# Kernel optimization log

Hardware: AMD Instinct MI355X
Metric: run time of the kernel (lower is better)

## Reference

```python
import jax, jax.numpy as jnp
import numpy as np
import math

HID = 1152
NH = 16
HD = HID // NH            # 72
P = 2
DEPTH = 4
MLP_M = int(2.0 / 3.0 * int(HID * 4.0))  # 3072 (SwiGLU inner)
FREQ = 256
NCLS = 1000
ROPE_THETA = 10000.0


def rms_norm(x, w, eps=1e-6):
    return x * jax.lax.rsqrt(jnp.mean(jnp.square(x), axis=-1, keepdims=True) + eps) * w


def rotate_half(x):
    # interleaved pairs (a, b) -> (-b, a)
    x2 = x.reshape(x.shape[:-1] + (x.shape[-1] // 2, 2))
    a, b = x2[..., 0], x2[..., 1]
    return jnp.stack((-b, a), axis=-1).reshape(x.shape)


def make_rope(S, head_dim, theta=ROPE_THETA):
    # VisionRotaryEmbedder: per-axis rope dim = head_dim//2, 2 spatial axes concat
    d = head_dim // 2
    f = 1.0 / theta ** (jnp.arange(0, d, 2)[: d // 2].astype(jnp.float32) / d)
    fr = jnp.arange(S, dtype=jnp.float32)[:, None] * f[None, :]   # [S, d//2]
    fr = jnp.repeat(fr, 2, axis=-1)                               # [S, d]
    grid = jnp.concatenate(
        [jnp.broadcast_to(fr[:, None, :], (S, S, d)),
         jnp.broadcast_to(fr[None, :, :], (S, S, d))], axis=-1)   # [S, S, head_dim]
    grid = grid.reshape(S * S, head_dim)
    return jnp.cos(grid), jnp.sin(grid)


def timestep_embedding(t, dim=FREQ, max_period=10000.0):
    half = dim // 2
    freqs = jnp.exp(-math.log(max_period) * jnp.arange(half, dtype=jnp.float32) / half)
    args = t[:, None].astype(jnp.float32) * freqs[None, :]
    return jnp.concatenate([jnp.cos(args), jnp.sin(args)], axis=-1)


def setup_inputs() -> dict:
    key = jax.random.key(0)
    ks = jax.random.split(key, 24)
    s = 0.02
    B, C, H, W = 2, 4, 64, 64
    d = {
        'x': jax.random.normal(ks[0], (B, C, H, W), jnp.float32),
        't': jax.random.uniform(ks[1], (B,), jnp.float32),
        'y': jax.random.randint(ks[2], (B,), 0, NCLS),
        'patch_w': jax.random.normal(ks[3], (P * P * C, HID), jnp.float32) * s,
        'patch_b': jnp.zeros((HID,), jnp.float32),
        't_w1': jax.random.normal(ks[4], (FREQ, HID), jnp.float32) * s,
        't_b1': jnp.zeros((HID,), jnp.float32),
        't_w2': jax.random.normal(ks[5], (HID, HID), jnp.float32) * s,
        't_b2': jnp.zeros((HID,), jnp.float32),
        'y_table': jax.random.normal(ks[6], (NCLS + 1, HID), jnp.float32) * s,
        'norm1_w': jnp.ones((DEPTH, HID), jnp.float32),
        'qkv_w': jax.random.normal(ks[7], (DEPTH, HID, 3 * HID), jnp.float32) * s,
        'qkv_b': jnp.zeros((DEPTH, 3 * HID), jnp.float32),
        'out_w': jax.random.normal(ks[8], (DEPTH, HID, HID), jnp.float32) * s,
        'out_b': jnp.zeros((DEPTH, HID), jnp.float32),
        'norm2_w': jnp.ones((DEPTH, HID), jnp.float32),
        'mlp_w12': jax.random.normal(ks[9], (DEPTH, HID, 2 * MLP_M), jnp.float32) * s,
        'mlp_b12': jnp.zeros((DEPTH, 2 * MLP_M), jnp.float32),
        'mlp_w3': jax.random.normal(ks[10], (DEPTH, MLP_M, HID), jnp.float32) * s,
        'mlp_b3': jnp.zeros((DEPTH, HID), jnp.float32),
        'adaln_w': jax.random.normal(ks[11], (DEPTH, HID, 4 * HID), jnp.float32) * s,
        'adaln_b': jnp.zeros((DEPTH, 4 * HID), jnp.float32),
        'fnorm_w': jnp.ones((HID,), jnp.float32),
        'fadaln_w': jax.random.normal(ks[12], (HID, 2 * HID), jnp.float32) * s,
        'fadaln_b': jnp.zeros((2 * HID,), jnp.float32),
        'flin_w': jax.random.normal(ks[13], (HID, P * P * C), jnp.float32) * s,
        'flin_b': jnp.zeros((P * P * C,), jnp.float32),
    }
    return d


def reference(x, t, y, patch_w, patch_b, t_w1, t_b1, t_w2, t_b2, y_table,
              norm1_w, qkv_w, qkv_b, out_w, out_b, norm2_w,
              mlp_w12, mlp_b12, mlp_w3, mlp_b3, adaln_w, adaln_b,
              fnorm_w, fadaln_w, fadaln_b, flin_w, flin_b):
    B, C, H, W = x.shape
    S = H // P
    L = S * S
    # patchify -> [B, L, P*P*C] -> linear embed
    tok = x.reshape(B, C, S, P, S, P).transpose(0, 2, 4, 3, 5, 1).reshape(B, L, P * P * C)
    h = tok @ patch_w + patch_b
    # conditioning: timestep MLP + class embedding
    temb = timestep_embedding(t)
    temb = jax.nn.silu(temb @ t_w1 + t_b1) @ t_w2 + t_b2
    c = temb + y_table[y]
    c_silu = jax.nn.silu(c)
    cos, sin = make_rope(S, HD)  # [L, HD]
    scale = 1.0 / math.sqrt(HD)

    def block(hx, p):
        n1w, qw, qb, ow, ob, n2w, w12, b12, w3, b3, aw, ab = p
        mod = c_silu @ aw + ab  # [B, 4*HID]
        s_msa, g_msa, s_mlp, g_mlp = jnp.split(mod, 4, axis=-1)
        hmod = rms_norm(hx, n1w) * (1.0 + s_msa[:, None, :])
        qkv = (hmod @ qw + qb).reshape(B, L, 3, NH, HD)
        qkv = jnp.swapaxes(qkv, 1, 3)  # [B, NH, 3, L, HD]
        q, k, v = qkv[:, :, 0], qkv[:, :, 1], qkv[:, :, 2]
        q = q * cos + rotate_half(q) * sin
        k = k * cos + rotate_half(k) * sin
        w = jax.nn.softmax(jnp.einsum('bhqd,bhkd->bhqk', q, k) * scale, axis=-1)
        o = jnp.einsum('bhqk,bhkd->bhqd', w, v)
        o = jnp.swapaxes(o, 1, 2).reshape(B, L, HID) @ ow + ob
        hx = hx + g_msa[:, None, :] * o
        hmod2 = rms_norm(hx, n2w) * (1.0 + s_mlp[:, None, :])
        x12 = hmod2 @ w12 + b12
        x1, x2 = jnp.split(x12, 2, axis=-1)
        m = (jax.nn.silu(x1) * x2) @ w3 + b3
        hx = hx + g_mlp[:, None, :] * m
        return hx, None

    h, _ = jax.lax.scan(block, h, (norm1_w, qkv_w, qkv_b, out_w, out_b, norm2_w,
                                   mlp_w12, mlp_b12, mlp_w3, mlp_b3, adaln_w, adaln_b))

    # final layer: shift+scale modulation then zero-init linear (random here)
    fmod = c_silu @ fadaln_w + fadaln_b
    shift, fscale = jnp.split(fmod, 2, axis=-1)
    hf = rms_norm(h, fnorm_w) * (1.0 + fscale[:, None, :]) + shift[:, None, :]
    out = hf @ flin_w + flin_b  # [B, L, P*P*C]
    out = out.reshape(B, S, S, P, P, C).transpose(0, 5, 1, 3, 2, 4).reshape(B, C, H, W)
    return out
```

## Files before the change

### kernel.cpp

```cpp
#include <hip/hip_runtime.h>
#include <hip/hip_bf16.h>

#define HIDN 1152
#define NHEAD 16
#define HDIM 72
#define LTOK 1024
#define MTOK 2048
#define MLPM 3072

typedef short bf16x8 __attribute__((ext_vector_type(8)));
typedef float f32x4 __attribute__((ext_vector_type(4)));

__device__ __forceinline__ void gload16(const void* g, void* l) {
    __builtin_amdgcn_global_load_lds(
        (const __attribute__((address_space(1))) void*)g,
        (__attribute__((address_space(3))) void*)l,
        16, 0, 0);
}

__global__ __launch_bounds__(256) void k_patch(const float* __restrict__ x,
        const float* __restrict__ pw, const float* __restrict__ pb,
        float* __restrict__ h) {
    int m = blockIdx.x;
    int b = m >> 10, l = m & 1023;
    int si = l >> 5, sj = l & 31;
    __shared__ float toks[16];
    int tid = threadIdx.x;
    if (tid < 16) {
        int pi = tid >> 3, pj = (tid >> 2) & 1, c = tid & 3;
        toks[tid] = x[((size_t)(b*4 + c)*64 + si*2 + pi)*64 + sj*2 + pj];
    }
    __syncthreads();
    for (int o = tid; o < HIDN; o += 256) {
        float acc = pb[o];
        #pragma unroll
        for (int kk = 0; kk < 16; ++kk) acc += toks[kk] * pw[kk*HIDN + o];
        h[(size_t)m*HIDN + o] = acc;
    }
}

__global__ __launch_bounds__(256) void k_temb1_v2(const float* __restrict__ t,
        const float* __restrict__ w1, const float* __restrict__ b1,
        float* __restrict__ temb1) {
    int jt = blockIdx.x, b = blockIdx.y;
    int tid = threadIdx.x;
    __shared__ float emb[256];
    __shared__ float red[128];
    float tv = t[b];
    if (tid < 128) { float f = __expf(-logf(10000.f) * (float)tid / 128.f);        emb[tid] = cosf(tv * f); }
    else           { float f = __expf(-logf(10000.f) * (float)(tid - 128) / 128.f); emb[tid] = sinf(tv * f); }
    __syncthreads();
    int o = jt*128 + (tid & 127), s = tid >> 7;
    float acc = 0.f;
    for (int k = s*128; k < s*128 + 128; ++k) acc += emb[k] * w1[(size_t)k*HIDN + o];
    if (s) red[tid & 127] = acc;
    __syncthreads();
    if (!s) {
        float v = acc + red[tid] + b1[o];
        temb1[b*HIDN + o] = v / (1.f + __expf(-v));
    }
}

__global__ __launch_bounds__(256) void k_csilu_s1(const float* __restrict__ temb1,
        const float* __restrict__ w2, float* __restrict__ csilup) {
    int jt = blockIdx.x, kz = blockIdx.y;
    int tid = threadIdx.x;
    __shared__ float t1s[2][288];
    __shared__ float red[2][128];
    for (int i = tid; i < 576; i += 256)
        t1s[i/288][i%288] = temb1[(i/288)*HIDN + kz*288 + (i%288)];
    __syncthreads();
    int o = jt*128 + (tid & 127), s = tid >> 7;
    float a0 = 0.f, a1 = 0.f;
    for (int i = s*144; i < s*144 + 144; ++i) {
        float wv = w2[(size_t)(kz*288 + i)*HIDN + o];
        a0 += t1s[0][i]*wv; a1 += t1s[1][i]*wv;
    }
    if (s) { red[0][tid & 127] = a0; red[1][tid & 127] = a1; }
    __syncthreads();
    if (!s) {
        csilup[(kz*2 + 0)*HIDN + o] = a0 + red[0][tid];
        csilup[(kz*2 + 1)*HIDN + o] = a1 + red[1][tid];
    }
}

__global__ __launch_bounds__(128) void k_csilu_s2(const float* __restrict__ csilup,
        const float* __restrict__ b2, const float* __restrict__ ytab,
        const int* __restrict__ y, float* __restrict__ csilu) {
    int o = blockIdx.x*128 + threadIdx.x;
    int b = blockIdx.y;
    float acc = b2[o] + ytab[(size_t)y[b]*HIDN + o];
    #pragma unroll
    for (int kz = 0; kz < 4; ++kz) acc += csilup[(kz*2 + b)*HIDN + o];
    csilu[b*HIDN + o] = acc / (1.f + __expf(-acc));
}

__global__ __launch_bounds__(256) void k_cond_s1(const float* __restrict__ csilu,
        const float* __restrict__ adaln_w, const float* __restrict__ fadaln_w,
        float* __restrict__ condp) {
    int ct = blockIdx.x, kz = blockIdx.y;
    int tid = threadIdx.x;
    int c0 = ct*128;
    const float* Wb; int rstride;
    if (c0 < 18432) { int d = c0/4608; Wb = adaln_w + (size_t)d*HIDN*4608 + (c0 % 4608); rstride = 4608; }
    else            { Wb = fadaln_w + (c0 - 18432); rstride = 2304; }
    __shared__ float cs[2][288];
    __shared__ float red[2][128];
    for (int i = tid; i < 576; i += 256)
        cs[i/288][i%288] = csilu[(i/288)*HIDN + kz*288 + (i%288)];
    __syncthreads();
    int o = tid & 127, s = tid >> 7;
    float a0 = 0.f, a1 = 0.f;
    for (int i = s*144; i < s*144 + 144; ++i) {
        float wv = Wb[(size_t)(kz*288 + i)*rstride + o];
        a0 += cs[0][i]*wv; a1 += cs[1][i]*wv;
    }
    if (s) { red[0][o] = a0; red[1][o] = a1; }
    __syncthreads();
    if (!s) {
        condp[((size_t)kz*2 + 0)*20736 + c0 + o] = a0 + red[0][o];
        condp[((size_t)kz*2 + 1)*20736 + c0 + o] = a1 + red[1][o];
    }
}

__global__ __launch_bounds__(256) void k_cond_s2(const float* __restrict__ condp,
        const float* __restrict__ adaln_b, const float* __restrict__ fadaln_b,
        float* __restrict__ modb, float* __restrict__ fmod) {
    int c = blockIdx.x*256 + threadIdx.x;
    int b = blockIdx.y;
    float acc = 0.f;
    #pragma unroll
    for (int kz = 0; kz < 4; ++kz) acc += condp[((size_t)kz*2 + b)*20736 + c];
    if (c < 18432) {
        int d = c/4608, j = c%4608;
        modb[((size_t)d*2 + b)*4608 + j] = acc + adaln_b[(size_t)d*4608 + j];
    } else {
        int j = c - 18432;
        fmod[(size_t)b*2304 + j] = acc + fadaln_b[j];
    }
}

__global__ __launch_bounds__(256) void k_rope(float* __restrict__ cosb, float* __restrict__ sinb) {
    int idx = blockIdx.x*256 + threadIdx.x;
    if (idx >= LTOK*HDIM) return;
    int l = idx / HDIM, dd = idx % HDIM;
    int i = l >> 5, j = l & 31;
    int pos = (dd < 36) ? i : j;
    int mm = ((dd < 36) ? dd : dd - 36) >> 1;
    float f = __expf(-logf(10000.f) * (float)mm / 18.f);
    float fr = (float)pos * f;
    cosb[idx] = cosf(fr);
    sinb[idx] = sinf(fr);
}

__global__ __launch_bounds__(256) void k_rms(const float* __restrict__ hx,
        const float* __restrict__ nw, const float* __restrict__ smod,
        __hip_bfloat16* __restrict__ outp) {
    int m = blockIdx.x; int b = m >> 10;
    int tid = threadIdx.x;
    const float* row = hx + (size_t)m*HIDN;
    float part = 0.f;
    for (int j = tid; j < HIDN; j += 256) { float v = row[j]; part += v*v; }
    for (int off = 32; off; off >>= 1) part += __shfl_xor(part, off);
    __shared__ float wsum[4];
    if ((tid & 63) == 0) wsum[tid >> 6] = part;
    __syncthreads();
    float rs = rsqrtf((wsum[0]+wsum[1]+wsum[2]+wsum[3]) * (1.f/HIDN) + 1e-6f);
    const float* sb = smod + (size_t)b*4608;
    __hip_bfloat16* orow = outp + (size_t)m*HIDN;
    for (int j = tid; j < HIDN; j += 256)
        orow[j] = __float2bfloat16(row[j] * rs * nw[j] * (1.f + sb[j]));
}

__global__ __launch_bounds__(256) void k_castT(const float* __restrict__ W,
        __hip_bfloat16* __restrict__ Wt, int K, int N) {
    __shared__ float tile[32][33];
    int n0 = blockIdx.x*32, k0 = blockIdx.y*32;
    int tx = threadIdx.x, ty = threadIdx.y;
    for (int i = ty; i < 32; i += 8)
        tile[i][tx] = W[(size_t)(k0+i)*N + n0 + tx];
    __syncthreads();
    for (int i = ty; i < 32; i += 8)
        Wt[(size_t)(n0+i)*K + k0 + tx] = __float2bfloat16(tile[tx][i]);
}

template<int EPI, typename OutT>
__global__ __launch_bounds__(256) void k_gemm_bf16(
        const __hip_bfloat16* __restrict__ A,
        const __hip_bfloat16* __restrict__ Wt,
        const float* __restrict__ bias,
        OutT* __restrict__ C, int M, int N, int K,
        const float* __restrict__ gate) {
    __shared__ __hip_bfloat16 Asm[128*64];
    __shared__ __hip_bfloat16 Bsm[128*64];
    int tid = threadIdx.x;
    int lane = tid & 63, w = tid >> 6;
    int wr = w >> 1, wc = w & 1;
    int m0 = blockIdx.y * 128, n0 = blockIdx.x * 128;
    f32x4 acc[4][4] = {};
    int lr = lane >> 3, ls = lane & 7;
    int swz = ls ^ (lr & 7);
    int x7 = lane & 7;
    const __hip_bfloat16* Ag = A  + (size_t)(m0 + lr)*K + swz*8;
    const __hip_bfloat16* Bg = Wt + (size_t)(n0 + lr)*K + swz*8;
    for (int k0 = 0; k0 < K; k0 += 64) {
        #pragma unroll
        for (int i = 0; i < 4; ++i) {
            int seg = w*4 + i;
            gload16(Ag + (size_t)(seg*8)*K + k0, (char*)Asm + seg*1024);
            gload16(Bg + (size_t)(seg*8)*K + k0, (char*)Bsm + seg*1024);
        }
        __syncthreads();
        #pragma unroll
        for (int kk = 0; kk < 2; ++kk) {
            bf16x8 af[4], bfr[4];
            #pragma unroll
            for (int m = 0; m < 4; ++m) {
                int row = wr*64 + m*16 + (lane&15);
                af[m] = *(const bf16x8*)(Asm + row*64 + (((kk*4 + (lane>>4)) ^ x7) * 8));
            }
            #pragma unroll
            for (int n = 0; n < 4; ++n) {
                int col = wc*64 + n*16 + (lane&15);
                bfr[n] = *(const bf16x8*)(Bsm + col*64 + (((kk*4 + (lane>>4)) ^ x7) * 8));
            }
            #pragma unroll
            for (int m = 0; m < 4; ++m)
                #pragma unroll
                for (int n = 0; n < 4; ++n)
                    acc[m][n] = __builtin_amdgcn_mfma_f32_16x16x32_bf16(af[m], bfr[n], acc[m][n], 0, 0, 0);
        }
        __syncthreads();
    }
    int r0 = (lane >> 4) * 4;
    int ccol = lane & 15;
    #pragma unroll
    for (int m = 0; m < 4; ++m) {
        #pragma unroll
        for (int rr = 0; rr < 4; ++rr) {
            int row = m0 + wr*64 + m*16 + r0 + rr;
            int bi = row >> 10;
            #pragma unroll
            for (int n = 0; n < 4; ++n) {
                int col = n0 + wc*64 + n*16 + ccol;
                float val = acc[m][n][rr] + bias[col];
                if (EPI == 0) {
                    C[(size_t)row*N + col] = (OutT)__float2bfloat16(val);
                } else {
                    ((float*)C)[(size_t)row*N + col] += gate[(size_t)bi*4608 + col] * val;
                }
            }
        }
    }
}

__global__ __launch_bounds__(256) void k_gemm64(
        const __hip_bfloat16* __restrict__ A,
        const __hip_bfloat16* __restrict__ Wt,
        const float* __restrict__ bias,
        float* __restrict__ C, int M, int N, int K,
        const float* __restrict__ gate) {
    __shared__ __hip_bfloat16 Asm[64*64];
    __shared__ __hip_bfloat16 Bsm[128*64];
    int tid = threadIdx.x;
    int lane = tid & 63, w = tid >> 6;
    int wr = w >> 1, wc = w & 1;
    int m0 = blockIdx.y * 64, n0 = blockIdx.x * 128;
    f32x4 acc[2][4] = {};
    int lr = lane >> 3, ls = lane & 7;
    int swz = ls ^ (lr & 7);
    int x7 = lane & 7;
    const __hip_bfloat16* Ag = A  + (size_t)(m0 + lr)*K + swz*8;
    const __hip_bfloat16* Bg = Wt + (size_t)(n0 + lr)*K + swz*8;
    for (int k0 = 0; k0 < K; k0 += 64) {
        #pragma unroll
        for (int i = 0; i < 2; ++i) {
            int seg = w*2 + i;
            gload16(Ag + (size_t)(seg*8)*K + k0, (char*)Asm + seg*1024);
        }
        #pragma unroll
        for (int i = 0; i < 4; ++i) {
            int seg = w*4 + i;
            gload16(Bg + (size_t)(seg*8)*K + k0, (char*)Bsm + seg*1024);
        }
        __syncthreads();
        #pragma unroll
        for (int kk = 0; kk < 2; ++kk) {
            bf16x8 af[2], bfr[4];
            #pragma unroll
            for (int m = 0; m < 2; ++m) {
                int row = wr*32 + m*16 + (lane&15);
                af[m] = *(const bf16x8*)(Asm + row*64 + (((kk*4 + (lane>>4)) ^ x7) * 8));
            }
            #pragma unroll
            for (int n = 0; n < 4; ++n) {
                int col = wc*64 + n*16 + (lane&15);
                bfr[n] = *(const bf16x8*)(Bsm + col*64 + (((kk*4 + (lane>>4)) ^ x7) * 8));
            }
            #pragma unroll
            for (int m = 0; m < 2; ++m)
                #pragma unroll
                for (int n = 0; n < 4; ++n)
                    acc[m][n] = __builtin_amdgcn_mfma_f32_16x16x32_bf16(af[m], bfr[n], acc[m][n], 0, 0, 0);
        }
        __syncthreads();
    }
    int r0 = (lane >> 4) * 4;
    int ccol = lane & 15;
    #pragma unroll
    for (int m = 0; m < 2; ++m) {
        #pragma unroll
        for (int rr = 0; rr < 4; ++rr) {
            int row = m0 + wr*32 + m*16 + r0 + rr;
            int bi = row >> 10;
            #pragma unroll
            for (int n = 0; n < 4; ++n) {
                int col = n0 + wc*64 + n*16 + ccol;
                float val = acc[m][n][rr] + bias[col];
                C[(size_t)row*N + col] += gate[(size_t)bi*4608 + col] * val;
            }
        }
    }
}

__global__ __launch_bounds__(256) void k_ropesplit(const __hip_bfloat16* __restrict__ qkv,
        const float* __restrict__ cosb, const float* __restrict__ sinb,
        __hip_bfloat16* __restrict__ q, __hip_bfloat16* __restrict__ k,
        __hip_bfloat16* __restrict__ v) {
    int idx = blockIdx.x*256 + threadIdx.x;
    if (idx >= 2*NHEAD*LTOK*36) return;
    int dp = idx % 36;
    int l  = (idx / 36) % LTOK;
    int h  = (idx / (36*LTOK)) % NHEAD;
    int b  = idx / (36*LTOK*NHEAD);
    int d0 = dp*2;
    size_t src = (size_t)(b*LTOK + l)*3456 + h*HDIM + d0;
    float qe = __bfloat162float(qkv[src]),        qo = __bfloat162float(qkv[src+1]);
    float ke = __bfloat162float(qkv[src+HIDN]),   ko = __bfloat162float(qkv[src+HIDN+1]);
    float ce = cosb[l*HDIM+d0], co = cosb[l*HDIM+d0+1];
    float se = sinb[l*HDIM+d0], so = sinb[l*HDIM+d0+1];
    size_t dst = (size_t)((b*NHEAD + h)*LTOK + l)*HDIM + d0;
    q[dst]   = __float2bfloat16(qe*ce - qo*se);
    q[dst+1] = __float2bfloat16(qo*co + qe*so);
    k[dst]   = __float2bfloat16(ke*ce - ko*se);
    k[dst+1] = __float2bfloat16(ko*co + ke*so);
    size_t vdst = ((size_t)(b*NHEAD + h)*HDIM + d0)*LTOK + l;
    v[vdst]        = qkv[src+2*HIDN];
    v[vdst+LTOK]   = qkv[src+2*HIDN+1];
}

__global__ __launch_bounds__(256) void k_attn_mfma(
        const __hip_bfloat16* __restrict__ q,
        const __hip_bfloat16* __restrict__ k,
        const __hip_bfloat16* __restrict__ vt,
        __hip_bfloat16* __restrict__ o) {
    int blk = blockIdx.x;
    int qt = blk & 15, h = (blk >> 4) & 15, b = blk >> 8;
    const float scale = 0.117851130f;
    __shared__ __hip_bfloat16 Ksm[2][64*72];
    __shared__ __hip_bfloat16 Vsm[2][72*64];
    __shared__ __hip_bfloat16 Psm[4][16*72];
    int tid = threadIdx.x, lane = tid & 63, w = tid >> 6;
    int l15 = lane & 15, g = lane >> 4;
    const __hip_bfloat16* qg = q  + ((size_t)(b*NHEAD + h)*LTOK + qt*64)*HDIM;
    const __hip_bfloat16* kg = k  + (size_t)(b*NHEAD + h)*LTOK*HDIM;
    const __hip_bfloat16* vg = vt + (size_t)(b*NHEAD + h)*HDIM*LTOK;
    const bf16x8 z = {};

    bf16x8 qf[3];
    {
        const __hip_bfloat16* qrow = qg + (w*16 + l15)*HDIM;
        qf[0] = *(const bf16x8*)(qrow + g*8);
        qf[1] = *(const bf16x8*)(qrow + 32 + g*8);
        qf[2] = (g == 0) ? *(const bf16x8*)(qrow + 64) : z;
    }
    int vsw  = ((lane & 7) ^ (lane >> 3)) * 8;
    int vrow = lane >> 3;

    f32x4 oacc[5] = {};
    float mold[4] = {-1e30f, -1e30f, -1e30f, -1e30f};
    float lsum[4] = {};

    {
        const __hip_bfloat16* ktg = kg;
        const __hip_bfloat16* vtg = vg;
        for (int s = w; s < 9; s += 4) {
            gload16(ktg + s*512 + lane*8, (char*)&Ksm[0][0] + s*1024);
            gload16(vtg + (size_t)(s*8 + vrow)*LTOK + vsw, (char*)&Vsm[0][0] + s*1024);
        }
    }
    __syncthreads();

    for (int kt2 = 0; kt2 < 16; ++kt2) {
        int cur = kt2 & 1;
        if (kt2 < 15) {
            const __hip_bfloat16* ktg = kg + (size_t)(kt2+1)*64*HDIM;
            const __hip_bfloat16* vtg = vg + (kt2+1)*64;
            for (int s = w; s < 9; s += 4) {
                gload16(ktg + s*512 + lane*8, (char*)&Ksm[cur^1][0] + s*1024);
                gload16(vtg + (size_t)(s*8 + vrow)*LTOK + vsw, (char*)&Vsm[cur^1][0] + s*1024);
            }
        }
        const __hip_bfloat16* Kc = Ksm[cur];
        const __hip_bfloat16* Vc = Vsm[cur];
        f32x4 st[4] = {};
        __builtin_amdgcn_s_setprio(1);
        #pragma unroll
        for (int t = 0; t < 4; ++t) {
            const __hip_bfloat16* krow = Kc + (t*16 + l15)*72;
            bf16x8 kf0 = *(const bf16x8*)(krow + g*8);
            bf16x8 kf1 = *(const bf16x8*)(krow + 32 + g*8);
            bf16x8 kf2 = (g == 0) ? *(const bf16x8*)(krow + 64) : z;
            st[t] = __builtin_amdgcn_mfma_f32_16x16x32_bf16(qf[0], kf0, st[t], 0, 0, 0);
            st[t] = __builtin_amdgcn_mfma_f32_16x16x32_bf16(qf[1], kf1, st[t], 0, 0, 0);
            st[t] = __builtin_amdgcn_mfma_f32_16x16x32_bf16(qf[2], kf2, st[t], 0, 0, 0);
        }
        __builtin_amdgcn_s_setprio(0);
        #pragma unroll
        for (int r = 0; r < 4; ++r) {
            float mt = fmaxf(fmaxf(st[0][r], st[1][r]), fmaxf(st[2][r], st[3][r]));
            mt = fmaxf(mt, __shfl_xor(mt, 1));
            mt = fmaxf(mt, __shfl_xor(mt, 2));
            mt = fmaxf(mt, __shfl_xor(mt, 4));
            mt = fmaxf(mt, __shfl_xor(mt, 8));
            float mn = fmaxf(mold[r], mt);
            float corr = __expf((mold[r] - mn) * scale);
            mold[r] = mn;
            lsum[r] *= corr;
            #pragma unroll
            for (int dt = 0; dt < 5; ++dt) oacc[dt][r] *= corr;
            float rs = 0.f;
            #pragma unroll
            for (int t = 0; t < 4; ++t) {
                float p = __expf((st[t][r] - mn) * scale);
                rs += p;
                Psm[w][(g*4 + r)*72 + t*16 + l15] = __float2bfloat16(p);
            }
            rs += __shfl_xor(rs, 1);
            rs += __shfl_xor(rs, 2);
            rs += __shfl_xor(rs, 4);
            rs += __shfl_xor(rs, 8);
            lsum[r] += rs;
        }
        bf16x8 pa0 = *(const bf16x8*)(&Psm[w][l15*72 + g*8]);
        bf16x8 pa1 = *(const bf16x8*)(&Psm[w][l15*72 + 32 + g*8]);
        int cswz = (l15 & 7)*8;
        __builtin_amdgcn_s_setprio(1);
        #pragma unroll
        for (int dt = 0; dt < 5; ++dt) {
            int row = dt*16 + l15;
            bool valid = (dt < 4) | (l15 < 8);
            bf16x8 vf0 = valid ? *(const bf16x8*)(Vc + row*64 + ((g*8) ^ cswz)) : z;
            bf16x8 vf1 = valid ? *(const bf16x8*)(Vc + row*64 + ((32 + g*8) ^ cswz)) : z;
            oacc[dt] = __builtin_amdgcn_mfma_f32_16x16x32_bf16(pa0, vf0, oacc[dt], 0, 0, 0);
            oacc[dt] = __builtin_amdgcn_mfma_f32_16x16x32_bf16(pa1, vf1, oacc[dt], 0, 0, 0);
        }
        __builtin_amdgcn_s_setprio(0);
        __syncthreads();
    }
    #pragma unroll
    for (int r = 0; r < 4; ++r) {
        float inv = 1.f / lsum[r];
        int row = qt*64 + w*16 + g*4 + r;
        __hip_bfloat16* op = o + ((size_t)b*LTOK + row)*HIDN + h*HDIM;
        #pragma unroll
        for (int dt = 0; dt < 5; ++dt) {
            int d = dt*16 + l15;
            if (d < HDIM) op[d] = __float2bfloat16(oacc[dt][r] * inv);
        }
    }
}

__global__ __launch_bounds__(256) void k_glu(const __hip_bfloat16* __restrict__ x12,
        __hip_bfloat16* __restrict__ mh) {
    int idx = blockIdx.x*256 + threadIdx.x;
    int m = idx / 384, jj = (idx % 384)*8;
    bf16x8 v1 = *(const bf16x8*)(x12 + (size_t)m*6144 + jj);
    bf16x8 v2 = *(const bf16x8*)(x12 + (size_t)m*6144 + MLPM + jj);
    bf16x8 ov;
    #pragma unroll
    for (int i = 0; i < 8; ++i) {
        short s1 = v1[i], s2 = v2[i];
        float x1 = __bfloat162float(*(__hip_bfloat16*)&s1);
        float x2 = __bfloat162float(*(__hip_bfloat16*)&s2);
        __hip_bfloat16 r = __float2bfloat16(x1 / (1.f + __expf(-x1)) * x2);
        ov[i] = *(short*)&r;
    }
    *(bf16x8*)(mh + (size_t)m*MLPM + jj) = ov;
}

__global__ __launch_bounds__(256) void k_final(const float* __restrict__ hx,
        const float* __restrict__ fnw, const float* __restrict__ fmod,
        const float* __restrict__ flw, const float* __restrict__ flb,
        float* __restrict__ out) {
    int m = blockIdx.x; int b = m >> 10, l = m & 1023;
    int tid = threadIdx.x;
    const float* row = hx + (size_t)m*HIDN;
    float part = 0.f;
    for (int j = tid; j < HIDN; j += 256) { float v2 = row[j]; part += v2*v2; }
    for (int off = 32; off; off >>= 1) part += __shfl_xor(part, off);
    __shared__ float wsum[4];
    __shared__ float hfs[HIDN];
    __shared__ float red[4][16];
    if ((tid & 63) == 0) wsum[tid >> 6] = part;
    __syncthreads();
    float rs = rsqrtf((wsum[0]+wsum[1]+wsum[2]+wsum[3]) * (1.f/HIDN) + 1e-6f);
    const float* fm = fmod + (size_t)b*2304;
    for (int j = tid; j < HIDN; j += 256)
        hfs[j] = row[j] * rs * fnw[j] * (1.f + fm[HIDN + j]) + fm[j];
    __syncthreads();
    float pacc[16] = {};
    for (int j = tid; j < HIDN; j += 256) {
        float hv = hfs[j];
        #pragma unroll
        for (int kk = 0; kk < 16; ++kk) pacc[kk] += hv * flw[j*16 + kk];
    }
    #pragma unroll
    for (int kk = 0; kk < 16; ++kk)
        for (int off = 32; off; off >>= 1) pacc[kk] += __shfl_xor(pacc[kk], off);
    if ((tid & 63) == 0) {
        int w = tid >> 6;
        #pragma unroll
        for (int kk = 0; kk < 16; ++kk) red[w][kk] = pacc[kk];
    }
    __syncthreads();
    if (tid < 16) {
        float val = red[0][tid] + red[1][tid] + red[2][tid] + red[3][tid] + flb[tid];
        int pi = tid >> 3, pj = (tid >> 2) & 1, c = tid & 3;
        int si = l >> 5, sj = l & 31;
        out[((size_t)(b*4 + c)*64 + si*2 + pi)*64 + sj*2 + pj] = val;
    }
}

extern "C" void kernel_launch(void* const* d_in, const int* in_sizes, int n_in,
                              void* d_out, int out_size, void* d_ws, size_t ws_size,
                              hipStream_t stream) {
    const float* x        = (const float*)d_in[0];
    const float* t        = (const float*)d_in[1];
    const int*   y        = (const int*)  d_in[2];
    const float* patch_w  = (const float*)d_in[3];
    const float* patch_b  = (const float*)d_in[4];
    const float* t_w1     = (const float*)d_in[5];
    const float* t_b1     = (const float*)d_in[6];
    const float* t_w2     = (const float*)d_in[7];
    const float* t_b2     = (const float*)d_in[8];
    const float* y_table  = (const float*)d_in[9];
    const float* norm1_w  = (const float*)d_in[10];
    const float* qkv_w    = (const float*)d_in[11];
    const float* qkv_b    = (const float*)d_in[12];
    const float* out_w    = (const float*)d_in[13];
    const float* out_b    = (const float*)d_in[14];
    const float* norm2_w  = (const float*)d_in[15];
    const float* mlp_w12  = (const float*)d_in[16];
    const float* mlp_b12  = (const float*)d_in[17];
    const float* mlp_w3   = (const float*)d_in[18];
    const float* mlp_b3   = (const float*)d_in[19];
    const float* adaln_w  = (const float*)d_in[20];
    const float* adaln_b  = (const float*)d_in[21];
    const float* fnorm_w  = (const float*)d_in[22];
    const float* fadaln_w = (const float*)d_in[23];
    const float* fadaln_b = (const float*)d_in[24];
    const float* flin_w   = (const float*)d_in[25];
    const float* flin_b   = (const float*)d_in[26];

    char* base = (char*)d_ws;
    float*          hx    = (float*)(base);
    __hip_bfloat16* qkvbf = (__hip_bfloat16*)(base +  9437184);
    __hip_bfloat16* qbf   = (__hip_bfloat16*)(base + 34603008);
    __hip_bfloat16* kbf   = (__hip_bfloat16*)(base + 39321600);
    __hip_bfloat16* vbf   = (__hip_bfloat16*)(base + 44040192);
    __hip_bfloat16* hbf   = (__hip_bfloat16*)(base + 48758784);
    __hip_bfloat16* mhbf  = qbf;
    __hip_bfloat16* wtb   = (__hip_bfloat16*)(base + 53477376);
    float* temb1 = (float*)(base + 85327872);
    float* csilu = (float*)(base + 85337088);
    float* modb  = (float*)(base + 85346304);
    float* fmod  = (float*)(base + 85493760);
    float* cosb  = (float*)(base + 85512192);
    float* sinb  = (float*)(base + 85807104);
    float* condp = (float*)(base + 86102016);
    float* csilup= (float*)(base + 86765568);

    __hip_bfloat16* wt_qkv = wtb;
    __hip_bfloat16* wt_out = wt_qkv + 3456*1152;
    __hip_bfloat16* wt_m12 = wt_out + 1152*1152;
    __hip_bfloat16* wt_m3  = wt_m12 + 6144*1152;

    k_patch<<<2048, 256, 0, stream>>>(x, patch_w, patch_b, hx);
    k_temb1_v2<<<dim3(9,2), 256, 0, stream>>>(t, t_w1, t_b1, temb1);
    k_csilu_s1<<<dim3(9,4), 256, 0, stream>>>(temb1, t_w2, csilup);
    k_csilu_s2<<<dim3(9,2), 128, 0, stream>>>(csilup, t_b2, y_table, y, csilu);
    k_cond_s1<<<dim3(162,4), 256, 0, stream>>>(csilu, adaln_w, fadaln_w, condp);
    k_cond_s2<<<dim3(81,2), 256, 0, stream>>>(condp, adaln_b, fadaln_b, modb, fmod);
    k_rope<<<288, 256, 0, stream>>>(cosb, sinb);

    for (int d = 0; d < 4; ++d) {
        const float* modd = modb + (size_t)d*2*4608;
        k_castT<<<dim3(108,36), dim3(32,8), 0, stream>>>(qkv_w  + (size_t)d*HIDN*3456, wt_qkv, HIDN, 3456);
        k_castT<<<dim3( 36,36), dim3(32,8), 0, stream>>>(out_w  + (size_t)d*HIDN*HIDN, wt_out, HIDN, HIDN);
        k_castT<<<dim3(192,36), dim3(32,8), 0, stream>>>(mlp_w12+ (size_t)d*HIDN*6144, wt_m12, HIDN, 6144);
        k_castT<<<dim3( 36,96), dim3(32,8), 0, stream>>>(mlp_w3 + (size_t)d*MLPM*HIDN, wt_m3,  MLPM, HIDN);

        k_rms<<<2048, 256, 0, stream>>>(hx, norm1_w + d*HIDN, modd + 0*HIDN, hbf);
        k_gemm_bf16<0, __hip_bfloat16><<<dim3(27,16), 256, 0, stream>>>(hbf, wt_qkv,
                qkv_b + d*3456, qkvbf, MTOK, 3456, HIDN, nullptr);
        k_ropesplit<<<4608, 256, 0, stream>>>(qkvbf, cosb, sinb, qbf, kbf, vbf);
        k_attn_mfma<<<512, 256, 0, stream>>>(qbf, kbf, vbf, hbf);
        k_gemm64<<<dim3(9,32), 256, 0, stream>>>(hbf, wt_out,
                out_b + d*HIDN, hx, MTOK, HIDN, HIDN, modd + 1*HIDN);
        k_rms<<<2048, 256, 0, stream>>>(hx, norm2_w + d*HIDN, modd + 2*HIDN, hbf);
        k_gemm_bf16<0, __hip_bfloat16><<<dim3(48,16), 256, 0, stream>>>(hbf, wt_m12,
                mlp_b12 + d*6144, qkvbf, MTOK, 6144, HIDN, nullptr);
        k_glu<<<3072, 256, 0, stream>>>(qkvbf, mhbf);
        k_gemm64<<<dim3(9,32), 256, 0, stream>>>(mhbf, wt_m3,
                mlp_b3 + d*HIDN, hx, MTOK, HIDN, MLPM, modd + 3*HIDN);
    }
    k_final<<<2048, 256, 0, stream>>>(hx, fnorm_w, fmod, flin_w, flin_b, (float*)d_out);
}
```

Baseline: 1.097 ms.

## Batch all weight transposes into one launch and fuse SwiGLU into GEMM

Replaces the sixteen per-layer cast/transpose launches with one kernel that converts all four layers' weights up front, using 64x64 tiles, float4 loads and 16-byte bf16 stores. The MLP w12 weights are interleaved so that x1 and x2 columns sit next to each other, which lets a new GEMM epilogue apply SiLU*gate through a lane shuffle and write the GLU output directly. This removes the separate k_glu pass and the write and re-read of the 6144-wide intermediate. The cost is a larger workspace holding every layer's transposed weights, with the scalar buffers moved to new offsets.

```diff
diff --git a/kernel.cpp b/kernel.cpp
--- a/kernel.cpp
+++ b/kernel.cpp
@@ -172,16 +172,43 @@
         orow[j] = __float2bfloat16(row[j] * rs * nw[j] * (1.f + sb[j]));
 }
 
-__global__ __launch_bounds__(256) void k_castT(const float* __restrict__ W,
-        __hip_bfloat16* __restrict__ Wt, int K, int N) {
-    __shared__ float tile[32][33];
-    int n0 = blockIdx.x*32, k0 = blockIdx.y*32;
-    int tx = threadIdx.x, ty = threadIdx.y;
-    for (int i = ty; i < 32; i += 8)
-        tile[i][tx] = W[(size_t)(k0+i)*N + n0 + tx];
-    __syncthreads();
-    for (int i = ty; i < 32; i += 8)
-        Wt[(size_t)(n0+i)*K + k0 + tx] = __float2bfloat16(tile[tx][i]);
+__global__ __launch_bounds__(256) void k_castT_all(
+        const float* __restrict__ qkv_w, const float* __restrict__ out_w,
+        const float* __restrict__ m12_w, const float* __restrict__ m3_w,
+        __hip_bfloat16* __restrict__ wtb) {
+    __shared__ float tile[64][65];
+    int bid = blockIdx.x;
+    int layer = bid / 3888, r = bid % 3888;
+    const float* W; __hip_bfloat16* Wt; int K, N, nt, t; bool glu = false;
+    __hip_bfloat16* bl = wtb + (size_t)layer*15925248;
+    if (r < 972)       { t = r;        nt = 54; K = 1152; N = 3456; W = qkv_w + (size_t)layer*K*N; Wt = bl; }
+    else if (r < 1296) { t = r - 972;  nt = 18; K = 1152; N = 1152; W = out_w + (size_t)layer*K*N; Wt = bl + 3981312; }
+    else if (r < 3024) { t = r - 1296; nt = 96; K = 1152; N = 6144; W = m12_w + (size_t)layer*K*N; Wt = bl + 5308416; glu = true; }
+    else               { t = r - 3024; nt = 18; K = 3072; N = 1152; W = m3_w  + (size_t)layer*K*N; Wt = bl + 12386304; }
+    int n0 = (t % nt)*64, k0 = (t / nt)*64;
+    int tid = threadIdx.x;
+    int rr = tid >> 4, c4 = (tid & 15)*4;
+    #pragma unroll
+    for (int p = 0; p < 4; ++p) {
+        int kk = p*16 + rr;
+        float4 v = *(const float4*)(W + (size_t)(k0+kk)*N + n0 + c4);
+        tile[kk][c4+0] = v.x; tile[kk][c4+1] = v.y; tile[kk][c4+2] = v.z; tile[kk][c4+3] = v.w;
+    }
+    __syncthreads();
+    int n = tid >> 3, kseg = tid & 7;
+    #pragma unroll
+    for (int p = 0; p < 2; ++p) {
+        int nn = n + p*32;
+        bf16x8 o;
+        #pragma unroll
+        for (int j = 0; j < 8; ++j) {
+            __hip_bfloat16 hv = __float2bfloat16(tile[kseg*8 + j][nn]);
+            o[j] = *(short*)&hv;
+        }
+        int ng = n0 + nn;
+        int np = glu ? ((ng < 3072) ? 2*ng : 2*(ng - 3072) + 1) : ng;
+        *(bf16x8*)(Wt + (size_t)np*K + k0 + kseg*8) = o;
+    }
 }
 
 template<int EPI, typename OutT>
@@ -243,11 +270,19 @@
             #pragma unroll
             for (int n = 0; n < 4; ++n) {
                 int col = n0 + wc*64 + n*16 + ccol;
-                float val = acc[m][n][rr] + bias[col];
                 if (EPI == 0) {
+                    float val = acc[m][n][rr] + bias[col];
                     C[(size_t)row*N + col] = (OutT)__float2bfloat16(val);
+                } else if (EPI == 1) {
+                    float val = acc[m][n][rr] + bias[col];
+                    ((float*)C)[(size_t)row*N + col] += gate[(size_t)bi*4608 + col] * val;
                 } else {
-                    ((float*)C)[(size_t)row*N + col] += gate[(size_t)bi*4608 + col] * val;
+                    float val = acc[m][n][rr] + bias[(col & 1) ? 3072 + (col >> 1) : (col >> 1)];
+                    float other = __shfl_xor(val, 1);
+                    if (!(lane & 1)) {
+                        float res = val / (1.f + __expf(-val)) * other;
+                        ((__hip_bfloat16*)C)[(size_t)row*(N>>1) + (col>>1)] = __float2bfloat16(res);
+                    }
                 }
             }
         }
@@ -469,24 +504,6 @@
             if (d < HDIM) op[d] = __float2bfloat16(oacc[dt][r] * inv);
         }
     }
-}
-
-__global__ __launch_bounds__(256) void k_glu(const __hip_bfloat16* __restrict__ x12,
-        __hip_bfloat16* __restrict__ mh) {
-    int idx = blockIdx.x*256 + threadIdx.x;
-    int m = idx / 384, jj = (idx % 384)*8;
-    bf16x8 v1 = *(const bf16x8*)(x12 + (size_t)m*6144 + jj);
-    bf16x8 v2 = *(const bf16x8*)(x12 + (size_t)m*6144 + MLPM + jj);
-    bf16x8 ov;
-    #pragma unroll
-    for (int i = 0; i < 8; ++i) {
-        short s1 = v1[i], s2 = v2[i];
-        float x1 = __bfloat162float(*(__hip_bfloat16*)&s1);
-        float x2 = __bfloat162float(*(__hip_bfloat16*)&s2);
-        __hip_bfloat16 r = __float2bfloat16(x1 / (1.f + __expf(-x1)) * x2);
-        ov[i] = *(short*)&r;
-    }
-    *(bf16x8*)(mh + (size_t)m*MLPM + jj) = ov;
 }
 
 __global__ __launch_bounds__(256) void k_final(const float* __restrict__ hx,
@@ -572,19 +589,14 @@
     __hip_bfloat16* hbf   = (__hip_bfloat16*)(base + 48758784);
     __hip_bfloat16* mhbf  = qbf;
     __hip_bfloat16* wtb   = (__hip_bfloat16*)(base + 53477376);
-    float* temb1 = (float*)(base + 85327872);
-    float* csilu = (float*)(base + 85337088);
-    float* modb  = (float*)(base + 85346304);
-    float* fmod  = (float*)(base + 85493760);
-    float* cosb  = (float*)(base + 85512192);
-    float* sinb  = (float*)(base + 85807104);
-    float* condp = (float*)(base + 86102016);
-    float* csilup= (float*)(base + 86765568);
-
-    __hip_bfloat16* wt_qkv = wtb;
-    __hip_bfloat16* wt_out = wt_qkv + 3456*1152;
-    __hip_bfloat16* wt_m12 = wt_out + 1152*1152;
-    __hip_bfloat16* wt_m3  = wt_m12 + 6144*1152;
+    float* temb1 = (float*)(base + 180879360);
+    float* csilu = (float*)(base + 180888576);
+    float* modb  = (float*)(base + 180897792);
+    float* fmod  = (float*)(base + 181045248);
+    float* cosb  = (float*)(base + 181063680);
+    float* sinb  = (float*)(base + 181358592);
+    float* condp = (float*)(base + 181653504);
+    float* csilup= (float*)(base + 182317056);
 
     k_patch<<<2048, 256, 0, stream>>>(x, patch_w, patch_b, hx);
     k_temb1_v2<<<dim3(9,2), 256, 0, stream>>>(t, t_w1, t_b1, temb1);
@@ -593,13 +605,15 @@
     k_cond_s1<<<dim3(162,4), 256, 0, stream>>>(csilu, adaln_w, fadaln_w, condp);
     k_cond_s2<<<dim3(81,2), 256, 0, stream>>>(condp, adaln_b, fadaln_b, modb, fmod);
     k_rope<<<288, 256, 0, stream>>>(cosb, sinb);
+    k_castT_all<<<15552, 256, 0, stream>>>(qkv_w, out_w, mlp_w12, mlp_w3, wtb);
 
     for (int d = 0; d < 4; ++d) {
         const float* modd = modb + (size_t)d*2*4608;
-        k_castT<<<dim3(108,36), dim3(32,8), 0, stream>>>(qkv_w  + (size_t)d*HIDN*3456, wt_qkv, HIDN, 3456);
-        k_castT<<<dim3( 36,36), dim3(32,8), 0, stream>>>(out_w  + (size_t)d*HIDN*HIDN, wt_out, HIDN, HIDN);
-        k_castT<<<dim3(192,36), dim3(32,8), 0, stream>>>(mlp_w12+ (size_t)d*HIDN*6144, wt_m12, HIDN, 6144);
-        k_castT<<<dim3( 36,96), dim3(32,8), 0, stream>>>(mlp_w3 + (size_t)d*MLPM*HIDN, wt_m3,  MLPM, HIDN);
+        __hip_bfloat16* wl = wtb + (size_t)d*15925248;
+        __hip_bfloat16* wt_qkv = wl;
+        __hip_bfloat16* wt_out = wl + 3981312;
+        __hip_bfloat16* wt_m12 = wl + 5308416;
+        __hip_bfloat16* wt_m3  = wl + 12386304;
 
         k_rms<<<2048, 256, 0, stream>>>(hx, norm1_w + d*HIDN, modd + 0*HIDN, hbf);
         k_gemm_bf16<0, __hip_bfloat16><<<dim3(27,16), 256, 0, stream>>>(hbf, wt_qkv,
@@ -609,9 +623,8 @@
         k_gemm64<<<dim3(9,32), 256, 0, stream>>>(hbf, wt_out,
                 out_b + d*HIDN, hx, MTOK, HIDN, HIDN, modd + 1*HIDN);
         k_rms<<<2048, 256, 0, stream>>>(hx, norm2_w + d*HIDN, modd + 2*HIDN, hbf);
-        k_gemm_bf16<0, __hip_bfloat16><<<dim3(48,16), 256, 0, stream>>>(hbf, wt_m12,
-                mlp_b12 + d*6144, qkvbf, MTOK, 6144, HIDN, nullptr);
-        k_glu<<<3072, 256, 0, stream>>>(qkvbf, mhbf);
+        k_gemm_bf16<2, __hip_bfloat16><<<dim3(48,16), 256, 0, stream>>>(hbf, wt_m12,
+                mlp_b12 + d*6144, mhbf, MTOK, 6144, HIDN, nullptr);
         k_gemm64<<<dim3(9,32), 256, 0, stream>>>(mhbf, wt_m3,
                 mlp_b3 + d*HIDN, hx, MTOK, HIDN, MLPM, modd + 3*HIDN);
     }
```

Measured after the change: 1.034 ms. -5.8%, faster.
